# Kernel optimization log

Hardware: AMD Instinct MI355X
Metric: run time of the kernel (lower is better)

The kernel has to match this reference:

```python
import jax, jax.numpy as jnp
import numpy as np

K = 5  # spline kernel size per dim (dim=3 -> 125 kernels)
NS = [20000, 5000, 1280, 320, 80, 32, 16]
ES = [320000, 80000, 20480, 5120, 1280, 512]
NF = [2, 16, 32, 64, 128, 128, 128]

_BITS = jnp.array([[(b >> d) & 1 for d in range(3)] for b in range(8)], dtype=jnp.int32)  # [8,3]
_STRIDES = jnp.array([1, K, K * K], dtype=jnp.int32)


def spline_conv(x, edge_index, pseudo, W, root, bias):
    """SplineConv, dim=3, kernel_size=5, degree-1 open B-splines, mean aggregation.
    x: [N,Cin], edge_index: [2,E], pseudo: [E,3] in [0,1], W: [125,Cin,Cout]."""
    N, Cin = x.shape
    src, dst = edge_index[0], edge_index[1]
    p = pseudo * (K - 1)                                  # [E,3]
    k0 = jnp.clip(jnp.floor(p), 0.0, K - 2)
    frac = p - k0                                         # [E,3]
    k0 = k0.astype(jnp.int32)
    # degree-1 basis: 2^3 = 8 active kernel corners per edge
    w = jnp.where(_BITS[None] == 1, frac[:, None, :], 1.0 - frac[:, None, :])  # [E,8,3]
    wprod = jnp.prod(w, axis=-1)                          # [E,8]
    kidx = jnp.sum((k0[:, None, :] + _BITS[None]) * _STRIDES, axis=-1)         # [E,8]
    xj = x[src]                                           # gather [E,Cin]
    # scatter weighted source features into (dst node, kernel) buckets
    seg = (dst[:, None] * (K ** 3) + kidx).reshape(-1)    # [E*8]
    contrib = (wprod[..., None] * xj[:, None, :]).reshape(-1, Cin)
    A = jax.ops.segment_sum(contrib, seg, num_segments=N * K ** 3).reshape(N, K ** 3, Cin)
    out = jnp.einsum('nki,kio->no', A, W)                 # [N,Cout]
    deg = jax.ops.segment_sum(jnp.ones(src.shape[0], x.dtype), dst, num_segments=N)
    out = out / jnp.maximum(deg, 1.0)[:, None]            # mean aggregation
    return out + x @ root + bias                          # root weight + bias


def _forward(x, eis, eas, Ps, Ws, Rs, bs):
    for l in range(6):
        h = jax.nn.elu(spline_conv(x, eis[l], eas[l], Ws[l], Rs[l], bs[l]))
        x = Ps[l].T @ h                                   # pool to coarser mesh
    return jnp.max(x, axis=0)[None, :]                    # AdaptiveMaxPool1d(1) over nodes -> [1,128]


def setup_inputs() -> dict:
    key = jax.random.key(0)
    ks = iter(jax.random.split(key, 64))
    inp = {"x": jax.random.normal(next(ks), (NS[0], NF[0]), jnp.float32)}
    for l in range(6):
        inp[f"ei{l}"] = jax.random.randint(next(ks), (2, ES[l]), 0, NS[l], dtype=jnp.int32)
        inp[f"ea{l}"] = jax.random.uniform(next(ks), (ES[l], 3), jnp.float32)
    pnames = ["P01", "P12", "P23", "P34", "P45", "P56"]
    for l, pn in enumerate(pnames):
        inp[pn] = jax.random.normal(next(ks), (NS[l], NS[l + 1]), jnp.float32) * (NS[l] ** -0.5)
    for l in range(6):
        cin, cout = NF[l], NF[l + 1]
        inp[f"W{l+1}"] = jax.random.normal(next(ks), (K ** 3, cin, cout), jnp.float32) * 0.05
        inp[f"R{l+1}"] = jax.random.normal(next(ks), (cin, cout), jnp.float32) * (cin ** -0.5)
        inp[f"b{l+1}"] = jnp.zeros((cout,), jnp.float32)
    return inp


def reference(x, ei0, ea0, ei1, ea1, ei2, ea2, ei3, ea3, ei4, ea4, ei5, ea5,
              P01, P12, P23, P34, P45, P56,
              W1, R1, b1, W2, R2, b2, W3, R3, b3,
              W4, R4, b4, W5, R5, b5, W6, R6, b6):
    eis = [ei0, ei1, ei2, ei3, ei4, ei5]
    eas = [ea0, ea1, ea2, ea3, ea4, ea5]
    Ps = [P01, P12, P23, P34, P45, P56]
    Ws = [W1, W2, W3, W4, W5, W6]
    Rs = [R1, R2, R3, R4, R5, R6]
    bs = [b1, b2, b3, b4, b5, b6]
    return _forward(x, eis, eas, Ps, Ws, Rs, bs)
```

## Files before the change

kernel.cpp:

```cpp
#include <hip/hip_runtime.h>
#include <math.h>

#define NKER 125

__global__ __launch_bounds__(256) void hist_kernel(const int* __restrict__ ei,
                                                   int* __restrict__ hist, int E) {
  int e = blockIdx.x * 256 + threadIdx.x;
  if (e < E) atomicAdd(&hist[ei[E + e]], 1);
}

__global__ __launch_bounds__(1024) void scan6_kernel(int* __restrict__ hist,
                                                     int* __restrict__ start,
                                                     int* __restrict__ cursor) {
  static const int histOff[6] = {0, 20000, 25000, 26280, 26600, 26680};
  static const int startOff[6] = {0, 20001, 25002, 26283, 26604, 26685};
  static const int Nl[6] = {20000, 5000, 1280, 320, 80, 32};
  __shared__ int ps[1024];
  int b = blockIdx.x;
  int* h = hist + histOff[b];
  int* s = start + startOff[b];
  int* c = cursor + histOff[b];
  int N = Nl[b];
  int t = threadIdx.x;
  int chunk = (N + 1023) / 1024;
  int lo = min(N, t * chunk), hi = min(N, lo + chunk);
  int sum = 0;
  for (int i = lo; i < hi; i++) sum += h[i];
  ps[t] = sum;
  __syncthreads();
  for (int off = 1; off < 1024; off <<= 1) {
    int v = (t >= off) ? ps[t - off] : 0;
    __syncthreads();
    ps[t] += v;
    __syncthreads();
  }
  int base = (t == 0) ? 0 : ps[t - 1];
  for (int i = lo; i < hi; i++) {
    int hv = h[i];
    s[i] = base;
    c[i] = base;
    base += hv;
  }
  if (t == 1023) s[N] = ps[1023];
}

__global__ __launch_bounds__(256) void reorder_kernel(
    const int* __restrict__ ei, const float* __restrict__ ea,
    int* __restrict__ cursor, int* __restrict__ srcS, int* __restrict__ kpkS,
    float* __restrict__ frS, int E) {
  int e = blockIdx.x * 256 + threadIdx.x;
  if (e >= E) return;
  int src = ei[e];
  int dst = ei[E + e];
  int kpk = 0;
  float f[3];
#pragma unroll
  for (int d = 0; d < 3; d++) {
    float p = ea[e * 3 + d] * 4.0f;
    float kf = fminf(fmaxf(floorf(p), 0.0f), 3.0f);
    f[d] = p - kf;
    kpk |= ((int)kf) << (4 * d);
  }
  int pos = atomicAdd(&cursor[dst], 1);
  srcS[pos] = src;
  kpkS[pos] = kpk;
  frS[pos * 3 + 0] = f[0];
  frS[pos * 3 + 1] = f[1];
  frS[pos * 3 + 2] = f[2];
}

template <int CINSH, int G, int KDIM, int KSG, int NT>
__global__ __launch_bounds__(NT) void build2_kernel(
    const int* __restrict__ start, const int* __restrict__ srcS,
    const int* __restrict__ kpkS, const float* __restrict__ frS,
    const float* __restrict__ x, float* __restrict__ A) {
  __shared__ float rows[G * KDIM];
  const int Cin = 1 << CINSH;
  int tid = threadIdx.x;
  int n0 = blockIdx.x * G;
  for (int t = tid; t < G * KDIM / 4; t += NT)
    ((float4*)rows)[t] = make_float4(0.0f, 0.0f, 0.0f, 0.0f);
  __syncthreads();
  int nl = tid >> CINSH;
  int ci = tid & (Cin - 1);
  int n = n0 + nl;
  int e0 = start[n], e1 = start[n + 1];
  float* row = rows + nl * KDIM + ci;
  for (int e = e0; e < e1; e++) {
    int src = srcS[e];
    int kpk = kpkS[e];
    float f0 = frS[3 * e], f1 = frS[3 * e + 1], f2 = frS[3 * e + 2];
    float xv = x[((size_t)src << CINSH) + ci];
    float g0 = 1.0f - f0, g1 = 1.0f - f1, g2 = 1.0f - f2;
    int kb = (kpk & 15) + 5 * ((kpk >> 4) & 15) + 25 * ((kpk >> 8) & 15);
    float* rb = row + (kb << CINSH);
    rb[0]              += (g0 * g1 * g2) * xv;
    rb[1 << CINSH]     += (f0 * g1 * g2) * xv;
    rb[5 << CINSH]     += (g0 * f1 * g2) * xv;
    rb[6 << CINSH]     += (f0 * f1 * g2) * xv;
    rb[25 << CINSH]    += (g0 * g1 * f2) * xv;
    rb[26 << CINSH]    += (f0 * g1 * f2) * xv;
    rb[30 << CINSH]    += (g0 * f1 * f2) * xv;
    rb[31 << CINSH]    += (f0 * f1 * f2) * xv;
  }
  __syncthreads();
  const int RQ = KSG / 4;
  for (int t = tid; t < G * RQ; t += NT) {
    int r = t / RQ, c4 = t % RQ;
    int c = c4 * 4;
    float4 v = make_float4(0.0f, 0.0f, 0.0f, 0.0f);
    if (c < KDIM) v = *(const float4*)&rows[r * KDIM + c];
    ((float4*)&A[(size_t)(n0 + r) * KSG])[c4] = v;
  }
}

__global__ __launch_bounds__(64) void build2_l0_kernel(
    const int* __restrict__ start, const int* __restrict__ srcS,
    const int* __restrict__ kpkS, const float* __restrict__ frS,
    const float* __restrict__ x, float* __restrict__ A, int N) {
  __shared__ float rows[64 * 254];
  int tid = threadIdx.x;
  int n0 = blockIdx.x * 64;
  for (int t = tid; t < 64 * 254 / 4; t += 64)
    ((float4*)rows)[t] = make_float4(0.0f, 0.0f, 0.0f, 0.0f);
  __syncthreads();
  int n = n0 + tid;
  if (n < N) {
    int e0 = start[n], e1 = start[n + 1];
    float* row = rows + tid * 254;
    for (int e = e0; e < e1; e++) {
      int src = srcS[e];
      int kpk = kpkS[e];
      float f0 = frS[3 * e], f1 = frS[3 * e + 1], f2 = frS[3 * e + 2];
      float2 xv = *(const float2*)&x[(size_t)src * 2];
      float g0 = 1.0f - f0, g1 = 1.0f - f1, g2 = 1.0f - f2;
      int kb = (kpk & 15) + 5 * ((kpk >> 4) & 15) + 25 * ((kpk >> 8) & 15);
      float2* rb = (float2*)(row + kb * 2);
      float w;
#define CORNER(off, expr)                                         \
      {                                                           \
        w = (expr);                                               \
        float2 v = rb[off];                                       \
        v.x = fmaf(w, xv.x, v.x); v.y = fmaf(w, xv.y, v.y);       \
        rb[off] = v;                                              \
      }
      CORNER(0,  g0 * g1 * g2)
      CORNER(1,  f0 * g1 * g2)
      CORNER(5,  g0 * f1 * g2)
      CORNER(6,  f0 * f1 * g2)
      CORNER(25, g0 * g1 * f2)
      CORNER(26, f0 * g1 * f2)
      CORNER(30, g0 * f1 * f2)
      CORNER(31, f0 * f1 * f2)
#undef CORNER
    }
  }
  __syncthreads();
  for (int it = 0; it < 64; it++) {
    int nn = n0 + it;
    if (nn >= N) break;
    int c = tid * 4;
    float4 v = make_float4(0.0f, 0.0f, 0.0f, 0.0f);
    if (tid < 63) v = *(const float4*)&rows[it * 254 + c];
    ((float4*)&A[(size_t)nn * 256])[tid] = v;
  }
}

template <int BM, int COUT, int NT>
__global__ __launch_bounds__(NT) void gemm3_kernel(
    const float* __restrict__ A, const float* __restrict__ W,
    float* __restrict__ gpart, int M, int Kdim, int KS, int ktiles) {
  const int BK = 32;
  __shared__ float At[BK][BM + 4];
  __shared__ float Wl[BK][COUT];
  const int TC = COUT / 4;
  int tid = threadIdx.x;
  int tc = tid % TC;
  int tr = tid / TC;
  int m0 = blockIdx.x * BM;
  int kbeg = blockIdx.y * ktiles * BK;
  int kend = min(KS, kbeg + ktiles * BK);
  float ar[4][4];
#pragma unroll
  for (int i = 0; i < 4; i++)
#pragma unroll
    for (int j = 0; j < 4; j++) ar[i][j] = 0.0f;

  for (int k0 = kbeg; k0 < kend; k0 += BK) {
    for (int t = tid; t < BM * (BK / 4); t += NT) {
      int c4 = t % (BK / 4), r = t / (BK / 4);
      int m = m0 + r;
      float4 v = make_float4(0.0f, 0.0f, 0.0f, 0.0f);
      if (m < M) v = *(const float4*)&A[(size_t)m * KS + k0 + c4 * 4];
      At[c4 * 4 + 0][r] = v.x; At[c4 * 4 + 1][r] = v.y;
      At[c4 * 4 + 2][r] = v.z; At[c4 * 4 + 3][r] = v.w;
    }
    int kleft = Kdim - k0;
    if (kleft >= BK) {
      for (int t = tid; t < BK * COUT / 4; t += NT)
        ((float4*)&Wl[0][0])[t] = ((const float4*)&W[(size_t)k0 * COUT])[t];
    } else {
      for (int t = tid; t < BK * COUT; t += NT) {
        int kk = t / COUT, o = t % COUT;
        Wl[kk][o] = (kk < kleft) ? W[(size_t)(k0 + kk) * COUT + o] : 0.0f;
      }
    }
    __syncthreads();
#pragma unroll
    for (int kk = 0; kk < BK; kk++) {
      float4 a = *(const float4*)&At[kk][tr * 4];
      float4 w = *(const float4*)&Wl[kk][tc * 4];
      float av[4] = {a.x, a.y, a.z, a.w};
      float wv[4] = {w.x, w.y, w.z, w.w};
#pragma unroll
      for (int i = 0; i < 4; i++)
#pragma unroll
        for (int j = 0; j < 4; j++)
          ar[i][j] = fmaf(av[i], wv[j], ar[i][j]);
    }
    __syncthreads();
  }
  float* gp = gpart + ((size_t)blockIdx.y * M) * COUT + tc * 4;
#pragma unroll
  for (int i = 0; i < 4; i++) {
    int m = m0 + tr * 4 + i;
    if (m < M)
      *(float4*)(gp + (size_t)m * COUT) =
          make_float4(ar[i][0], ar[i][1], ar[i][2], ar[i][3]);
  }
}

__global__ __launch_bounds__(256) void epilogue_kernel(
    const float* __restrict__ gpart, const int* __restrict__ degI,
    const float* __restrict__ x, const float* __restrict__ R,
    const float* __restrict__ b, float* __restrict__ h,
    int N, int Cin, int coutShift, int kchunks) {
  int tid = blockIdx.x * 256 + threadIdx.x;
  int Cout = 1 << coutShift;
  if (tid >= (N << coutShift)) return;
  int n = tid >> coutShift;
  int o = tid & (Cout - 1);
  size_t stride = (size_t)N << coutShift;
  float s = 0.0f;
  for (int c = 0; c < kchunks; c++) s += gpart[(size_t)c * stride + tid];
  s /= (float)max(degI[n], 1);
  float r = b[o];
  const float* xr = &x[n * Cin];
  for (int i = 0; i < Cin; i++) r = fmaf(xr[i], R[i * Cout + o], r);
  float v = s + r;
  h[tid] = v > 0.0f ? v : expm1f(v);
}

#define FMA4(c, pj, h) \
  c.x = fmaf(pj, h.x, c.x); c.y = fmaf(pj, h.y, c.y); \
  c.z = fmaf(pj, h.z, c.z); c.w = fmaf(pj, h.w, c.w);

template <int COUT, int OPT>
__global__ __launch_bounds__(256) void pool5b_kernel(
    const float* __restrict__ P, const float* __restrict__ h,
    float* __restrict__ partial, int Nsrc, int Nnext, int chunk, int items) {
  extern __shared__ float hs[];
  int c = blockIdx.y;
  int n0 = c * chunk;
  int n1 = min(Nsrc, n0 + chunk);
  int len = n1 - n0;
  for (int t = threadIdx.x; t < len * (COUT / 4); t += 256)
    ((float4*)hs)[t] = ((const float4*)&h[(size_t)n0 * COUT])[t];
  __syncthreads();
  int item = blockIdx.x * 256 + threadIdx.x;
  if (item >= items) return;
  int nj4 = Nnext >> 2;
  int j0 = (item % nj4) << 2;
  int o0 = (item / nj4) * OPT;
  const float4 z = make_float4(0.0f, 0.0f, 0.0f, 0.0f);
  float4 c00 = z, c01 = z, c02 = z, c03 = z;
  float4 c10 = z, c11 = z, c12 = z, c13 = z;
  float4 c20 = z, c21 = z, c22 = z, c23 = z;
  float4 c30 = z, c31 = z, c32 = z, c33 = z;
  const float* Pb = P + j0;

#define USTEP(pv, nn)                                                    \
  {                                                                      \
    const float4* hr = (const float4*)&hs[(nn) * COUT + o0];             \
    float4 h0 = hr[0], h1 = hr[1];                                       \
    FMA4(c00, pv.x, h0) FMA4(c01, pv.x, h1)                              \
    FMA4(c10, pv.y, h0) FMA4(c11, pv.y, h1)                              \
    FMA4(c20, pv.z, h0) FMA4(c21, pv.z, h1)                              \
    FMA4(c30, pv.w, h0) FMA4(c31, pv.w, h1)                              \
    if constexpr (OPT == 16) {                                           \
      float4 h2 = hr[2], h3 = hr[3];                                     \
      FMA4(c02, pv.x, h2) FMA4(c03, pv.x, h3)                            \
      FMA4(c12, pv.y, h2) FMA4(c13, pv.y, h3)                            \
      FMA4(c22, pv.z, h2) FMA4(c23, pv.z, h3)                            \
      FMA4(c32, pv.w, h2) FMA4(c33, pv.w, h3)                            \
    }                                                                    \
  }

  int n = 0;
  for (; n + 4 <= len; n += 4) {
    float4 pv0 = *(const float4*)&Pb[(size_t)(n0 + n + 0) * Nnext];
    float4 pv1 = *(const float4*)&Pb[(size_t)(n0 + n + 1) * Nnext];
    float4 pv2 = *(const float4*)&Pb[(size_t)(n0 + n + 2) * Nnext];
    float4 pv3 = *(const float4*)&Pb[(size_t)(n0 + n + 3) * Nnext];
    USTEP(pv0, n + 0)
    USTEP(pv1, n + 1)
    USTEP(pv2, n + 2)
    USTEP(pv3, n + 3)
  }
  for (; n < len; n++) {
    float4 pv = *(const float4*)&Pb[(size_t)(n0 + n) * Nnext];
    USTEP(pv, n)
  }
#undef USTEP

  float* pp = partial + ((size_t)c * Nnext + j0) * COUT + o0;
  *(float4*)(pp + 0 * COUT + 0) = c00;
  *(float4*)(pp + 0 * COUT + 4) = c01;
  *(float4*)(pp + 1 * COUT + 0) = c10;
  *(float4*)(pp + 1 * COUT + 4) = c11;
  *(float4*)(pp + 2 * COUT + 0) = c20;
  *(float4*)(pp + 2 * COUT + 4) = c21;
  *(float4*)(pp + 3 * COUT + 0) = c30;
  *(float4*)(pp + 3 * COUT + 4) = c31;
  if constexpr (OPT == 16) {
    *(float4*)(pp + 0 * COUT + 8)  = c02;
    *(float4*)(pp + 0 * COUT + 12) = c03;
    *(float4*)(pp + 1 * COUT + 8)  = c12;
    *(float4*)(pp + 1 * COUT + 12) = c13;
    *(float4*)(pp + 2 * COUT + 8)  = c22;
    *(float4*)(pp + 2 * COUT + 12) = c23;
    *(float4*)(pp + 3 * COUT + 8)  = c32;
    *(float4*)(pp + 3 * COUT + 12) = c33;
  }
}

__global__ __launch_bounds__(256) void preduce_kernel(
    const float* __restrict__ partial, float* __restrict__ xnext,
    int NnCout, int chunks) {
  int i = blockIdx.x * 256 + threadIdx.x;
  if (i >= NnCout) return;
  float s = 0.0f;
  for (int c = 0; c < chunks; c++) s += partial[(size_t)c * NnCout + i];
  xnext[i] = s;
}

__global__ __launch_bounds__(128) void max_kernel(const float* __restrict__ x6,
                                                  float* __restrict__ out) {
  int o = threadIdx.x;
  float m = -3.0e38f;
  for (int n = 0; n < 16; n++) m = fmaxf(m, x6[n * 128 + o]);
  out[o] = m;
}

extern "C" void kernel_launch(void* const* d_in, const int* in_sizes, int n_in,
                              void* d_out, int out_size, void* d_ws, size_t ws_size,
                              hipStream_t stream) {
  static const int NSh[7] = {20000, 5000, 1280, 320, 80, 32, 16};
  static const int ESh[6] = {320000, 80000, 20480, 5120, 1280, 512};
  static const int NFh[7] = {2, 16, 32, 64, 128, 128, 128};
  static const int cinSh[6]  = {1, 4, 5, 6, 7, 7};
  static const int coutSh[6] = {4, 5, 6, 7, 7, 7};
  static const int KSt[6] = {256, 2016, 4000, 8000, 16000, 16000};
  static const int kchunksTab[6] = {4, 8, 16, 32, 64, 128};
  static const int ktilesTab[6]  = {2, 8, 8, 8, 8, 4};
  static const int poolChunksTab[6] = {120, 64, 16, 8, 4, 2};
  static const int histOff[6] = {0, 20000, 25000, 26280, 26600, 26680};
  static const int startOff[6] = {0, 20001, 25002, 26283, 26604, 26685};
  static const int Eoff[6] = {0, 320000, 400000, 420480, 425600, 426880};

  const float* x0 = (const float*)d_in[0];
  const int* ei[6];
  const float* ea[6];
  for (int l = 0; l < 6; l++) {
    ei[l] = (const int*)d_in[1 + 2 * l];
    ea[l] = (const float*)d_in[2 + 2 * l];
  }
  const float* Pm[6];
  for (int l = 0; l < 6; l++) Pm[l] = (const float*)d_in[13 + l];
  const float* Wt[6];
  const float* Rt[6];
  const float* bt[6];
  for (int l = 0; l < 6; l++) {
    Wt[l] = (const float*)d_in[19 + 3 * l];
    Rt[l] = (const float*)d_in[20 + 3 * l];
    bt[l] = (const float*)d_in[21 + 3 * l];
  }

  float* ws = (float*)d_ws;
  float* A     = ws;
  float* gpart = ws + 10150000;
  float* hbuf  = ws + 11500000;
  float* ppart = ws + 11900000;
  float* xA    = ws + 21600000;
  float* xB    = ws + 21700000;
  int* hist    = (int*)(ws + 21800000);
  int* startA  = (int*)(ws + 21830000);
  int* cursor  = (int*)(ws + 21860000);
  int* srcS    = (int*)(ws + 21890000);
  int* kpkS    = (int*)(ws + 22320000);
  float* frS   = ws + 22750000;

  hipMemsetAsync(hist, 0, 26712 * sizeof(int), stream);
  for (int l = 0; l < 6; l++)
    hist_kernel<<<(ESh[l] + 255) / 256, 256, 0, stream>>>(ei[l], hist + histOff[l], ESh[l]);
  scan6_kernel<<<6, 1024, 0, stream>>>(hist, startA, cursor);
  for (int l = 0; l < 6; l++)
    reorder_kernel<<<(ESh[l] + 255) / 256, 256, 0, stream>>>(
        ei[l], ea[l], cursor + histOff[l], srcS + Eoff[l], kpkS + Eoff[l],
        frS + 3 * (size_t)Eoff[l], ESh[l]);

  const float* cur = x0;
  for (int l = 0; l < 6; l++) {
    int N = NSh[l], Nn = NSh[l + 1], Cin = NFh[l], Cout = NFh[l + 1];
    int Kdim = NKER * Cin, KS = KSt[l];
    float* xnext = (l & 1) ? xB : xA;
    const int* st = startA + startOff[l];
    const int* ss = srcS + Eoff[l];
    const int* kk = kpkS + Eoff[l];
    const float* ff = frS + 3 * (size_t)Eoff[l];

    switch (l) {
      case 0: build2_l0_kernel<<<313, 64, 0, stream>>>(st, ss, kk, ff, cur, A, N); break;
      case 1: build2_kernel<4, 8, 2000, 2016, 128><<<625, 128, 0, stream>>>(st, ss, kk, ff, cur, A); break;
      case 2: build2_kernel<5, 4, 4000, 4000, 128><<<320, 128, 0, stream>>>(st, ss, kk, ff, cur, A); break;
      case 3: build2_kernel<6, 2, 8000, 8000, 128><<<160, 128, 0, stream>>>(st, ss, kk, ff, cur, A); break;
      case 4: build2_kernel<7, 1, 16000, 16000, 128><<<80, 128, 0, stream>>>(st, ss, kk, ff, cur, A); break;
      default: build2_kernel<7, 1, 16000, 16000, 128><<<32, 128, 0, stream>>>(st, ss, kk, ff, cur, A); break;
    }

    int kchunks = kchunksTab[l], ktiles = ktilesTab[l];
    switch (l) {
      case 0: {
        dim3 g((N + 127) / 128, kchunks);
        gemm3_kernel<128, 16, 128><<<g, 128, 0, stream>>>(A, Wt[l], gpart, N, Kdim, KS, ktiles);
        break;
      }
      case 1: {
        dim3 g((N + 127) / 128, kchunks);
        gemm3_kernel<128, 32, 256><<<g, 256, 0, stream>>>(A, Wt[l], gpart, N, Kdim, KS, ktiles);
        break;
      }
      case 2: {
        dim3 g((N + 63) / 64, kchunks);
        gemm3_kernel<64, 64, 256><<<g, 256, 0, stream>>>(A, Wt[l], gpart, N, Kdim, KS, ktiles);
        break;
      }
      default: {
        dim3 g((N + 31) / 32, kchunks);
        gemm3_kernel<32, 128, 256><<<g, 256, 0, stream>>>(A, Wt[l], gpart, N, Kdim, KS, ktiles);
        break;
      }
    }

    int ethreads = N << coutSh[l];
    epilogue_kernel<<<(ethreads + 255) / 256, 256, 0, stream>>>(
        gpart, hist + histOff[l], cur, Rt[l], bt[l], hbuf, N, Cin, coutSh[l], kchunks);

    int pc = poolChunksTab[l];
    int chunk = (N + pc - 1) / pc;
    size_t ldsB = (size_t)chunk * Cout * sizeof(float);
    int items, gx;
    switch (Cout) {
      case 16:
        items = (Nn >> 2) * 1;
        gx = (items + 255) / 256;
        pool5b_kernel<16, 16><<<dim3(gx, pc), 256, ldsB, stream>>>(Pm[l], hbuf, ppart, N, Nn, chunk, items);
        break;
      case 32:
        items = (Nn >> 2) * 2;
        gx = (items + 255) / 256;
        pool5b_kernel<32, 16><<<dim3(gx, pc), 256, ldsB, stream>>>(Pm[l], hbuf, ppart, N, Nn, chunk, items);
        break;
      case 64:
        items = (Nn >> 2) * 8;
        gx = (items + 255) / 256;
        pool5b_kernel<64, 8><<<dim3(gx, pc), 256, ldsB, stream>>>(Pm[l], hbuf, ppart, N, Nn, chunk, items);
        break;
      default:
        items = (Nn >> 2) * 16;
        gx = (items + 255) / 256;
        pool5b_kernel<128, 8><<<dim3(gx, pc), 256, ldsB, stream>>>(Pm[l], hbuf, ppart, N, Nn, chunk, items);
        break;
    }
    int NnCout = Nn << coutSh[l];
    preduce_kernel<<<(NnCout + 255) / 256, 256, 0, stream>>>(ppart, xnext, NnCout, pc);

    cur = xnext;
  }

  max_kernel<<<1, 128, 0, stream>>>(cur, (float*)d_out);
}
```

Baseline: 819.9 us.

## Merge per-level hist/reorder launches and split layer-0 build across channel threads

```diff
diff --git a/kernel.cpp b/kernel.cpp
--- a/kernel.cpp
+++ b/kernel.cpp
@@ -3,10 +3,18 @@
 
 #define NKER 125
 
-__global__ __launch_bounds__(256) void hist_kernel(const int* __restrict__ ei,
-                                                   int* __restrict__ hist, int E) {
-  int e = blockIdx.x * 256 + threadIdx.x;
-  if (e < E) atomicAdd(&hist[ei[E + e]], 1);
+struct Ptr6i { const int* p[6]; };
+struct Ptr6f { const float* p[6]; };
+
+__global__ __launch_bounds__(256) void hist_all_kernel(Ptr6i eis, int* __restrict__ hist) {
+  static const int EB[7] = {0, 1250, 1563, 1643, 1663, 1668, 1670};
+  static const int Es[6] = {320000, 80000, 20480, 5120, 1280, 512};
+  static const int hOff[6] = {0, 20000, 25000, 26280, 26600, 26680};
+  int b = blockIdx.x;
+  int l = 0;
+  while (b >= EB[l + 1]) l++;
+  int e = (b - EB[l]) * 256 + threadIdx.x;
+  if (e < Es[l]) atomicAdd(&hist[hOff[l] + eis.p[l][Es[l] + e]], 1);
 }
 
 __global__ __launch_bounds__(1024) void scan6_kernel(int* __restrict__ hist,
@@ -44,14 +52,22 @@
   if (t == 1023) s[N] = ps[1023];
 }
 
-__global__ __launch_bounds__(256) void reorder_kernel(
-    const int* __restrict__ ei, const float* __restrict__ ea,
-    int* __restrict__ cursor, int* __restrict__ srcS, int* __restrict__ kpkS,
-    float* __restrict__ frS, int E) {
-  int e = blockIdx.x * 256 + threadIdx.x;
-  if (e >= E) return;
+__global__ __launch_bounds__(256) void reorder_all_kernel(
+    Ptr6i eis, Ptr6f eas, int* __restrict__ cursor,
+    int* __restrict__ srcS, int* __restrict__ kpkS, float* __restrict__ frS) {
+  static const int EB[7] = {0, 1250, 1563, 1643, 1663, 1668, 1670};
+  static const int Es[6] = {320000, 80000, 20480, 5120, 1280, 512};
+  static const int hOff[6] = {0, 20000, 25000, 26280, 26600, 26680};
+  static const int EoffK[6] = {0, 320000, 400000, 420480, 425600, 426880};
+  int b = blockIdx.x;
+  int l = 0;
+  while (b >= EB[l + 1]) l++;
+  int e = (b - EB[l]) * 256 + threadIdx.x;
+  if (e >= Es[l]) return;
+  const int* ei = eis.p[l];
+  const float* ea = eas.p[l];
   int src = ei[e];
-  int dst = ei[E + e];
+  int dst = ei[Es[l] + e];
   int kpk = 0;
   float f[3];
 #pragma unroll
@@ -61,7 +77,7 @@
     f[d] = p - kf;
     kpk |= ((int)kf) << (4 * d);
   }
-  int pos = atomicAdd(&cursor[dst], 1);
+  int pos = EoffK[l] + atomicAdd(&cursor[hOff[l] + dst], 1);
   srcS[pos] = src;
   kpkS[pos] = kpk;
   frS[pos * 3 + 0] = f[0];
@@ -114,55 +130,49 @@
   }
 }
 
-__global__ __launch_bounds__(64) void build2_l0_kernel(
+__global__ __launch_bounds__(128) void build2_l0_kernel(
     const int* __restrict__ start, const int* __restrict__ srcS,
     const int* __restrict__ kpkS, const float* __restrict__ frS,
     const float* __restrict__ x, float* __restrict__ A, int N) {
   __shared__ float rows[64 * 254];
   int tid = threadIdx.x;
   int n0 = blockIdx.x * 64;
-  for (int t = tid; t < 64 * 254 / 4; t += 64)
+  for (int t = tid; t < 64 * 254 / 4; t += 128)
     ((float4*)rows)[t] = make_float4(0.0f, 0.0f, 0.0f, 0.0f);
   __syncthreads();
-  int n = n0 + tid;
+  int nl = tid >> 1;
+  int ci = tid & 1;
+  int n = n0 + nl;
   if (n < N) {
     int e0 = start[n], e1 = start[n + 1];
-    float* row = rows + tid * 254;
+    float* row = rows + nl * 254 + ci;
     for (int e = e0; e < e1; e++) {
       int src = srcS[e];
       int kpk = kpkS[e];
       float f0 = frS[3 * e], f1 = frS[3 * e + 1], f2 = frS[3 * e + 2];
-      float2 xv = *(const float2*)&x[(size_t)src * 2];
+      float xv = x[(size_t)src * 2 + ci];
       float g0 = 1.0f - f0, g1 = 1.0f - f1, g2 = 1.0f - f2;
       int kb = (kpk & 15) + 5 * ((kpk >> 4) & 15) + 25 * ((kpk >> 8) & 15);
-      float2* rb = (float2*)(row + kb * 2);
-      float w;
-#define CORNER(off, expr)                                         \
-      {                                                           \
-        w = (expr);                                               \
-        float2 v = rb[off];                                       \
-        v.x = fmaf(w, xv.x, v.x); v.y = fmaf(w, xv.y, v.y);       \
-        rb[off] = v;                                              \
-      }
-      CORNER(0,  g0 * g1 * g2)
-      CORNER(1,  f0 * g1 * g2)
-      CORNER(5,  g0 * f1 * g2)
-      CORNER(6,  f0 * f1 * g2)
-      CORNER(25, g0 * g1 * f2)
-      CORNER(26, f0 * g1 * f2)
-      CORNER(30, g0 * f1 * f2)
-      CORNER(31, f0 * f1 * f2)
-#undef CORNER
-    }
-  }
-  __syncthreads();
-  for (int it = 0; it < 64; it++) {
-    int nn = n0 + it;
-    if (nn >= N) break;
-    int c = tid * 4;
+      float* rb = row + kb * 2;
+      rb[0]  = fmaf(g0 * g1 * g2, xv, rb[0]);
+      rb[2]  = fmaf(f0 * g1 * g2, xv, rb[2]);
+      rb[10] = fmaf(g0 * f1 * g2, xv, rb[10]);
+      rb[12] = fmaf(f0 * f1 * g2, xv, rb[12]);
+      rb[50] = fmaf(g0 * g1 * f2, xv, rb[50]);
+      rb[52] = fmaf(f0 * g1 * f2, xv, rb[52]);
+      rb[60] = fmaf(g0 * f1 * f2, xv, rb[60]);
+      rb[62] = fmaf(f0 * f1 * f2, xv, rb[62]);
+    }
+  }
+  __syncthreads();
+  for (int it = 0; it < 32; it++) {
+    int sub = tid >> 6;
+    int c4 = tid & 63;
+    int nn = n0 + it * 2 + sub;
+    if (nn >= N) continue;
     float4 v = make_float4(0.0f, 0.0f, 0.0f, 0.0f);
-    if (tid < 63) v = *(const float4*)&rows[it * 254 + c];
-    ((float4*)&A[(size_t)nn * 256])[tid] = v;
+    if (c4 < 63) v = *(const float4*)&rows[(it * 2 + sub) * 254 + c4 * 4];
+    ((float4*)&A[(size_t)nn * 256])[c4] = v;
   }
 }
 
@@ -363,17 +373,17 @@
   static const int KSt[6] = {256, 2016, 4000, 8000, 16000, 16000};
   static const int kchunksTab[6] = {4, 8, 16, 32, 64, 128};
   static const int ktilesTab[6]  = {2, 8, 8, 8, 8, 4};
-  static const int poolChunksTab[6] = {120, 64, 16, 8, 4, 2};
+  static const int poolChunksTab[6] = {250, 80, 16, 8, 4, 2};
   static const int histOff[6] = {0, 20000, 25000, 26280, 26600, 26680};
   static const int startOff[6] = {0, 20001, 25002, 26283, 26604, 26685};
   static const int Eoff[6] = {0, 320000, 400000, 420480, 425600, 426880};
 
   const float* x0 = (const float*)d_in[0];
-  const int* ei[6];
-  const float* ea[6];
+  Ptr6i eis;
+  Ptr6f eas;
   for (int l = 0; l < 6; l++) {
-    ei[l] = (const int*)d_in[1 + 2 * l];
-    ea[l] = (const float*)d_in[2 + 2 * l];
+    eis.p[l] = (const int*)d_in[1 + 2 * l];
+    eas.p[l] = (const float*)d_in[2 + 2 * l];
   }
   const float* Pm[6];
   for (int l = 0; l < 6; l++) Pm[l] = (const float*)d_in[13 + l];
@@ -390,24 +400,20 @@
   float* A     = ws;
   float* gpart = ws + 10150000;
   float* hbuf  = ws + 11500000;
-  float* ppart = ws + 11900000;
-  float* xA    = ws + 21600000;
-  float* xB    = ws + 21700000;
-  int* hist    = (int*)(ws + 21800000);
-  int* startA  = (int*)(ws + 21830000);
-  int* cursor  = (int*)(ws + 21860000);
-  int* srcS    = (int*)(ws + 21890000);
-  int* kpkS    = (int*)(ws + 22320000);
-  float* frS   = ws + 22750000;
+  float* ppart = ws + 12000000;
+  float* xA    = ws + 32100000;
+  float* xB    = ws + 32200000;
+  int* hist    = (int*)(ws + 32300000);
+  int* startA  = (int*)(ws + 32330000);
+  int* cursor  = (int*)(ws + 32360000);
+  int* srcS    = (int*)(ws + 32390000);
+  int* kpkS    = (int*)(ws + 32900000);
+  float* frS   = ws + 33400000;
 
   hipMemsetAsync(hist, 0, 26712 * sizeof(int), stream);
-  for (int l = 0; l < 6; l++)
-    hist_kernel<<<(ESh[l] + 255) / 256, 256, 0, stream>>>(ei[l], hist + histOff[l], ESh[l]);
+  hist_all_kernel<<<1670, 256, 0, stream>>>(eis, hist);
   scan6_kernel<<<6, 1024, 0, stream>>>(hist, startA, cursor);
-  for (int l = 0; l < 6; l++)
-    reorder_kernel<<<(ESh[l] + 255) / 256, 256, 0, stream>>>(
-        ei[l], ea[l], cursor + histOff[l], srcS + Eoff[l], kpkS + Eoff[l],
-        frS + 3 * (size_t)Eoff[l], ESh[l]);
+  reorder_all_kernel<<<1670, 256, 0, stream>>>(eis, eas, cursor, srcS, kpkS, frS);
 
   const float* cur = x0;
   for (int l = 0; l < 6; l++) {
@@ -420,7 +426,7 @@
     const float* ff = frS + 3 * (size_t)Eoff[l];
 
     switch (l) {
-      case 0: build2_l0_kernel<<<313, 64, 0, stream>>>(st, ss, kk, ff, cur, A, N); break;
+      case 0: build2_l0_kernel<<<313, 128, 0, stream>>>(st, ss, kk, ff, cur, A, N); break;
       case 1: build2_kernel<4, 8, 2000, 2016, 128><<<625, 128, 0, stream>>>(st, ss, kk, ff, cur, A); break;
       case 2: build2_kernel<5, 4, 4000, 4000, 128><<<320, 128, 0, stream>>>(st, ss, kk, ff, cur, A); break;
       case 3: build2_kernel<6, 2, 8000, 8000, 128><<<160, 128, 0, stream>>>(st, ss, kk, ff, cur, A); break;
```

After: 823.4 us. No clear change (+0.4%).
